# Kernel tuning notes

Hardware: AMD Instinct MI355X
Metric: run time of the kernel (lower is better)

The kernel has to match this reference:

```python
import jax, jax.numpy as jnp
import numpy as np

H, F, E_SHARED, E_ROUTED, K = 1024, 4096, 1, 8, 2


def setup_inputs() -> dict:
    key = jax.random.key(0)
    ks = jax.random.split(key, 6)
    x = jax.random.normal(ks[0], (4, 2048, H), dtype=jnp.float32)
    s = 0.02
    shared_up = jax.random.normal(ks[1], (E_SHARED, H, F), dtype=jnp.float32) * s
    shared_down = jax.random.normal(ks[2], (E_SHARED, F, H), dtype=jnp.float32) * s
    routed_up = jax.random.normal(ks[3], (E_ROUTED, H, F), dtype=jnp.float32) * s
    routed_down = jax.random.normal(ks[4], (E_ROUTED, F, H), dtype=jnp.float32) * s
    router_w = jax.random.normal(ks[5], (H, E_ROUTED), dtype=jnp.float32) * s
    return {"x": x, "shared_up": shared_up, "shared_down": shared_down,
            "routed_up": routed_up, "routed_down": routed_down, "router_w": router_w}


def _expert(x, w_up, w_down):
    # ExpertBlock: down(gelu(up(x))), exact (erf) gelu as in torch F.gelu default
    h = jax.nn.gelu(jnp.einsum('bsh,hf->bsf', x, w_up), approximate=False)
    return jnp.einsum('bsf,fh->bsh', h, w_down)


def reference(x, shared_up, shared_down, routed_up, routed_down, router_w):
    # shared experts (always active)
    shared_out = jnp.zeros_like(x)
    for i in range(E_SHARED):
        shared_out = shared_out + _expert(x, shared_up[i], shared_down[i])

    # router: softmax over routed experts, then top-k gating
    probs = jax.nn.softmax(jnp.einsum('bsh,he->bse', x, router_w), axis=-1)
    top_k_prob, top_k_idx = jax.lax.top_k(probs, K)  # [B,S,K]
    # per-expert gate = sum of top-k probs assigned to that expert
    onehot = jax.nn.one_hot(top_k_idx, E_ROUTED, dtype=x.dtype)  # [B,S,K,E]
    gates = jnp.einsum('bsk,bske->bse', top_k_prob, onehot)      # [B,S,E]

    routed_out = jnp.zeros_like(x)
    for e in range(E_ROUTED):  # fixed small loop over experts
        y = _expert(x, routed_up[e], routed_down[e])
        routed_out = routed_out + gates[..., e:e + 1] * y

    return shared_out + routed_out + x
```

## Files before the change

### kernel.cpp

```cpp
#include <hip/hip_runtime.h>
#include <cstdint>
#include <cstddef>

#define HD 1024
#define FF 4096
#define TOK 8192
#define NSEG 9
#define ROWS_ROUTED (TOK*2)
#define ROWS_TOT (ROWS_ROUTED + TOK)

typedef __bf16 bf16;
typedef __bf16 bf16x8 __attribute__((ext_vector_type(8)));
typedef __bf16 bf16x4 __attribute__((ext_vector_type(4)));
typedef float  f32x4  __attribute__((ext_vector_type(4)));

__device__ __forceinline__ void stage16(const void* g, void* l) {
  __builtin_amdgcn_global_load_lds((const __attribute__((address_space(1))) void*)g,
                                   (__attribute__((address_space(3))) void*)l,
                                   16, 0, 0);
}

__device__ __forceinline__ unsigned short bf_bits(float v) {
  bf16 b = (bf16)v;
  return __builtin_bit_cast(unsigned short, b);
}

__device__ __forceinline__ int xcd_remap(int d) {
  return (((d >> 6) << 3) + (d & 7)) * 8 + ((d >> 3) & 7);
}

__global__ void k_init_meta(int* meta) {
  int t = threadIdx.x;
  if (t < 64) meta[t] = 0;
}

__global__ void k_convert_x(const float* __restrict__ x, bf16* __restrict__ xbf) {
  int i = blockIdx.x*256 + threadIdx.x;
  float4 v = reinterpret_cast<const float4*>(x)[i];
  ushort4 u;
  u.x = bf_bits(v.x); u.y = bf_bits(v.y); u.z = bf_bits(v.z); u.w = bf_bits(v.w);
  reinterpret_cast<ushort4*>(xbf)[i] = u;
}

__global__ void k_tcvt(const float* __restrict__ routed, const float* __restrict__ shared_,
                       bf16* __restrict__ dst, int R, int C) {
  int e = blockIdx.z;
  const float* src = (e < 8) ? (routed + (size_t)e*R*C) : shared_;
  bf16* d = dst + (size_t)e*R*C;
  __shared__ float lds[64][65];
  int r0 = blockIdx.y*64, c0 = blockIdx.x*64;
  int t = threadIdx.x;
  int tr = t>>4, tc4 = (t&15)*4;
  #pragma unroll
  for (int i=0;i<4;i++) {
    float4 v = *reinterpret_cast<const float4*>(src + (size_t)(r0+tr+i*16)*C + c0 + tc4);
    lds[tr+i*16][tc4+0]=v.x; lds[tr+i*16][tc4+1]=v.y;
    lds[tr+i*16][tc4+2]=v.z; lds[tr+i*16][tc4+3]=v.w;
  }
  __syncthreads();
  #pragma unroll
  for (int i=0;i<4;i++) {
    int oc = tr + i*16;
    ushort4 u;
    u.x = bf_bits(lds[tc4+0][oc]);
    u.y = bf_bits(lds[tc4+1][oc]);
    u.z = bf_bits(lds[tc4+2][oc]);
    u.w = bf_bits(lds[tc4+3][oc]);
    *reinterpret_cast<ushort4*>(d + (size_t)(c0+oc)*R + r0 + tc4) = u;
  }
}

__global__ void k_router(const float* __restrict__ x, const float* __restrict__ rw,
                         int* __restrict__ rtE, float* __restrict__ rtG,
                         int* __restrict__ meta) {
  __shared__ float rwl[HD*8];
  int t = threadIdx.x;
  for (int i=t;i<HD*8/4;i+=256)
    reinterpret_cast<float4*>(rwl)[i] = reinterpret_cast<const float4*>(rw)[i];
  __syncthreads();
  int wv = t>>6, lane = t&63;
  int tk = blockIdx.x*4 + wv;
  const float* xr = x + (size_t)tk*HD;
  float a[8] = {0,0,0,0,0,0,0,0};
  for (int i=0;i<HD/64;i++) {
    int h = lane + i*64;
    float xv = xr[h];
    const float* r = rwl + h*8;
    #pragma unroll
    for (int e=0;e<8;e++) a[e] = fmaf(xv, r[e], a[e]);
  }
  #pragma unroll
  for (int e=0;e<8;e++) {
    for (int s=32;s>0;s>>=1) a[e] += __shfl_xor(a[e], s, 64);
  }
  if (lane==0) {
    float mx = a[0];
    #pragma unroll
    for (int e=1;e<8;e++) mx = fmaxf(mx, a[e]);
    float p[8]; float den = 0.f;
    #pragma unroll
    for (int e=0;e<8;e++) { p[e] = expf(a[e]-mx); den += p[e]; }
    int i0 = 0;
    #pragma unroll
    for (int e=1;e<8;e++) if (p[e] > p[i0]) i0 = e;
    int i1 = (i0==0)?1:0;
    #pragma unroll
    for (int e=0;e<8;e++) if (e!=i0 && p[e] > p[i1]) i1 = e;
    float inv = 1.f/den;
    rtE[tk*2] = i0; rtE[tk*2+1] = i1;
    rtG[tk*2] = p[i0]*inv; rtG[tk*2+1] = p[i1]*inv;
    atomicAdd(&meta[i0], 1);
    atomicAdd(&meta[i1], 1);
  }
}

__global__ void k_prefix(int* meta) {
  if (threadIdx.x == 0) {
    int off = 0;
    for (int e=0;e<8;e++) { meta[16+e] = off; meta[32+e] = meta[e]; off += meta[e]; }
    meta[16+8] = ROWS_ROUTED;
    meta[32+8] = TOK;
  }
}

__global__ void k_scatter(const int* __restrict__ rtE, const float* __restrict__ rtG,
                          int* __restrict__ meta, int* __restrict__ tok,
                          float* __restrict__ gate, int* __restrict__ trow) {
  int t = blockIdx.x*256 + threadIdx.x;
  int e0 = rtE[t*2], e1 = rtE[t*2+1];
  float g0 = rtG[t*2], g1 = rtG[t*2+1];
  int p0 = atomicAdd(&meta[8+e0], 1);
  int r0 = meta[16+e0] + p0;
  tok[r0] = t; gate[r0] = g0; trow[t*2] = r0;
  int p1 = atomicAdd(&meta[8+e1], 1);
  int r1 = meta[16+e1] + p1;
  tok[r1] = t; gate[r1] = g1; trow[t*2+1] = r1;
  tok[ROWS_ROUTED + t] = t; gate[ROWS_ROUTED + t] = 1.0f;
}

__global__ void k_combine(const float* __restrict__ x, const bf16* __restrict__ dbuf,
                          const int* __restrict__ trow, float* __restrict__ out) {
  int tkn = blockIdx.x;
  int t = threadIdx.x;
  int r0 = trow[tkn*2], r1 = trow[tkn*2+1];
  int h = t*4;
  float4 xv = *reinterpret_cast<const float4*>(x + (size_t)tkn*HD + h);
  bf16x4 a = *reinterpret_cast<const bf16x4*>(dbuf + (size_t)(ROWS_ROUTED+tkn)*HD + h);
  bf16x4 b = *reinterpret_cast<const bf16x4*>(dbuf + (size_t)r0*HD + h);
  bf16x4 c = *reinterpret_cast<const bf16x4*>(dbuf + (size_t)r1*HD + h);
  float4 o;
  o.x = xv.x + (float)a[0] + (float)b[0] + (float)c[0];
  o.y = xv.y + (float)a[1] + (float)b[1] + (float)c[1];
  o.z = xv.z + (float)a[2] + (float)b[2] + (float)c[2];
  o.w = xv.w + (float)a[3] + (float)b[3] + (float)c[3];
  *reinterpret_cast<float4*>(out + (size_t)tkn*HD + h) = o;
}


#define NKU (HD/32)
#define NKD (FF/32)

__global__ __launch_bounds__(256,3) void k_gemm_up(
    const bf16* __restrict__ xbf, const bf16* __restrict__ wupT,
    bf16* __restrict__ hbuf, const int* __restrict__ tok,
    const int* __restrict__ meta)
{
  int bx = xcd_remap(blockIdx.x);
  int seg = bx >> 11;
  int rem = bx & 2047;
  int mt = rem >> 5, nt = rem & 31;
  int rows = (seg<8)? meta[32+seg] : TOK;
  if (mt*128 >= rows) return;
  int segoff = meta[16+seg];
  int rowbase = mt*128;

  __shared__ __align__(16) bf16 Alds[3][128*32];
  __shared__ __align__(16) bf16 Blds[3][128*32];

  const int t = threadIdx.x;
  const int lane = t & 63, w = t >> 6;

  int lr0 = t>>2, lr1 = 64 + (t>>2);
  int gr0 = rowbase + lr0; if (gr0 >= rows) gr0 = rowbase;
  int gr1 = rowbase + lr1; if (gr1 >= rows) gr1 = rowbase;
  int tok0 = tok[segoff + gr0], tok1 = tok[segoff + gr1];
  int kswz = ((t&3) ^ ((t>>3)&3)) * 8;
  const bf16* gA0 = xbf + (size_t)tok0*HD + kswz;
  const bf16* gA1 = xbf + (size_t)tok1*HD + kswz;
  const bf16* wb = wupT + (size_t)seg*FF*HD;
  int f0 = nt*128;
  const bf16* gB0 = wb + (size_t)(f0 + lr0)*HD + kswz;
  const bf16* gB1 = wb + (size_t)(f0 + lr1)*HD + kswz;

  char* AldsB = (char*)Alds; char* BldsB = (char*)Blds;
  const int stoff = w*1024;

  const int slotb = ((lane>>4) ^ (((lane&15)>>1)&3)) * 16;
  const int Afo = ((w>>1)*64 + (lane&15))*64 + slotb;
  const int Bfo = ((w&1)*64 + (lane&15))*64 + slotb;

  f32x4 acc[4][4] = {};

  stage16(gA0,    AldsB + stoff); stage16(gA1,    AldsB + 4096 + stoff);
  stage16(gB0,    BldsB + stoff); stage16(gB1,    BldsB + 4096 + stoff);
  stage16(gA0+32, AldsB + 8192 + stoff); stage16(gA1+32, AldsB + 12288 + stoff);
  stage16(gB0+32, BldsB + 8192 + stoff); stage16(gB1+32, BldsB + 12288 + stoff);
  __syncthreads();

  int cur = 0;
  for (int kt = 0; kt < NKU; ++kt) {
    if (kt + 2 < NKU) {
      int st = (cur >= 1) ? cur - 1 : 2;
      int ko = (kt+2)*32;
      char* an = AldsB + st*8192; char* bn = BldsB + st*8192;
      stage16(gA0+ko, an + stoff); stage16(gA1+ko, an + 4096 + stoff);
      stage16(gB0+ko, bn + stoff); stage16(gB1+ko, bn + 4096 + stoff);
    }
    const char* Ab = AldsB + cur*8192 + Afo;
    const char* Bb = BldsB + cur*8192 + Bfo;
    bf16x8 af[4], bfr[4];
    #pragma unroll
    for (int m=0;m<4;m++) af[m]  = *reinterpret_cast<const bf16x8*>(Ab + m*1024);
    #pragma unroll
    for (int n=0;n<4;n++) bfr[n] = *reinterpret_cast<const bf16x8*>(Bb + n*1024);
    __builtin_amdgcn_s_setprio(1);
    #pragma unroll
    for (int m=0;m<4;m++)
      #pragma unroll
      for (int n=0;n<4;n++)
        acc[m][n] = __builtin_amdgcn_mfma_f32_16x16x32_bf16(bfr[n], af[m], acc[m][n], 0,0,0);
    __builtin_amdgcn_s_setprio(0);
    if (kt + 2 < NKU)      asm volatile("s_waitcnt vmcnt(8)" ::: "memory");
    else if (kt + 1 < NKU) asm volatile("s_waitcnt vmcnt(0)" ::: "memory");
    if (kt + 1 < NKU) __builtin_amdgcn_s_barrier();
    cur = (cur >= 2) ? 0 : cur + 1;
  }

  const int lrm = lane&15, lq = lane>>4;
  #pragma unroll
  for (int m=0;m<4;m++) {
    int rl = (w>>1)*64 + m*16 + lrm;
    int gr = rowbase + rl;
    if (gr >= rows) continue;
    bf16* hrow = hbuf + (size_t)(segoff+gr)*FF + nt*128 + (w&1)*64 + lq*4;
    #pragma unroll
    for (int n=0;n<4;n++) {
      bf16x4 u;
      #pragma unroll
      for (int j=0;j<4;j++) {
        float v = acc[m][n][j];
        v = 0.5f*v*(1.0f + erff(v*0.70710678118654752f));
        u[j] = (bf16)v;
      }
      *reinterpret_cast<bf16x4*>(hrow + n*16) = u;
    }
  }
}

__global__ __launch_bounds__(256,3) void k_gemm_down(
    const bf16* __restrict__ hbuf, const bf16* __restrict__ wdnT,
    bf16* __restrict__ dbuf, const float* __restrict__ gate,
    const int* __restrict__ meta)
{
  int bx = xcd_remap(blockIdx.x);
  int seg = bx >> 9;
  int rem = bx & 511;
  int mt = rem >> 3, nt = rem & 7;
  int rows = (seg<8)? meta[32+seg] : TOK;
  if (mt*128 >= rows) return;
  int segoff = meta[16+seg];
  int rowbase = mt*128;

  __shared__ __align__(16) bf16 Alds[3][128*32];
  __shared__ __align__(16) bf16 Blds[3][128*32];
  __shared__ float gateL[128];

  const int t = threadIdx.x;
  const int lane = t & 63, w = t >> 6;

  if (t < 128) {
    int gr = rowbase + t; if (gr >= rows) gr = rows - 1;
    gateL[t] = gate[segoff + gr];
  }

  int lr0 = t>>2, lr1 = 64 + (t>>2);
  int kswz = ((t&3) ^ ((t>>3)&3)) * 8;
  const bf16* gA0 = hbuf + (size_t)(segoff + rowbase + lr0)*FF + kswz;
  const bf16* gA1 = hbuf + (size_t)(segoff + rowbase + lr1)*FF + kswz;
  const bf16* wb = wdnT + (size_t)seg*HD*FF;
  int h0 = nt*128;
  const bf16* gB0 = wb + (size_t)(h0 + lr0)*FF + kswz;
  const bf16* gB1 = wb + (size_t)(h0 + lr1)*FF + kswz;

  char* AldsB = (char*)Alds; char* BldsB = (char*)Blds;
  const int stoff = w*1024;

  const int slotb = ((lane>>4) ^ (((lane&15)>>1)&3)) * 16;
  const int Afo = ((w>>1)*64 + (lane&15))*64 + slotb;
  const int Bfo = ((w&1)*64 + (lane&15))*64 + slotb;

  f32x4 acc[4][4] = {};

  stage16(gA0,    AldsB + stoff); stage16(gA1,    AldsB + 4096 + stoff);
  stage16(gB0,    BldsB + stoff); stage16(gB1,    BldsB + 4096 + stoff);
  stage16(gA0+32, AldsB + 8192 + stoff); stage16(gA1+32, AldsB + 12288 + stoff);
  stage16(gB0+32, BldsB + 8192 + stoff); stage16(gB1+32, BldsB + 12288 + stoff);
  __syncthreads();

  int cur = 0;
  for (int kt = 0; kt < NKD; ++kt) {
    if (kt + 2 < NKD) {
      int st = (cur >= 1) ? cur - 1 : 2;
      int ko = (kt+2)*32;
      char* an = AldsB + st*8192; char* bn = BldsB + st*8192;
      stage16(gA0+ko, an + stoff); stage16(gA1+ko, an + 4096 + stoff);
      stage16(gB0+ko, bn + stoff); stage16(gB1+ko, bn + 4096 + stoff);
    }
    const char* Ab = AldsB + cur*8192 + Afo;
    const char* Bb = BldsB + cur*8192 + Bfo;
    bf16x8 af[4], bfr[4];
    #pragma unroll
    for (int m=0;m<4;m++) af[m]  = *reinterpret_cast<const bf16x8*>(Ab + m*1024);
    #pragma unroll
    for (int n=0;n<4;n++) bfr[n] = *reinterpret_cast<const bf16x8*>(Bb + n*1024);
    __builtin_amdgcn_s_setprio(1);
    #pragma unroll
    for (int m=0;m<4;m++)
      #pragma unroll
      for (int n=0;n<4;n++)
        acc[m][n] = __builtin_amdgcn_mfma_f32_16x16x32_bf16(bfr[n], af[m], acc[m][n], 0,0,0);
    __builtin_amdgcn_s_setprio(0);
    if (kt + 2 < NKD)      asm volatile("s_waitcnt vmcnt(8)" ::: "memory");
    else if (kt + 1 < NKD) asm volatile("s_waitcnt vmcnt(0)" ::: "memory");
    if (kt + 1 < NKD) __builtin_amdgcn_s_barrier();
    cur = (cur >= 2) ? 0 : cur + 1;
  }

  const int lrm = lane&15, lq = lane>>4;
  #pragma unroll
  for (int m=0;m<4;m++) {
    int rl = (w>>1)*64 + m*16 + lrm;
    int gr = rowbase + rl;
    if (gr >= rows) continue;
    float g = gateL[rl];
    bf16* drow = dbuf + (size_t)(segoff+gr)*HD + nt*128 + (w&1)*64 + lq*4;
    #pragma unroll
    for (int n=0;n<4;n++) {
      bf16x4 u;
      #pragma unroll
      for (int j=0;j<4;j++) u[j] = (bf16)(acc[m][n][j]*g);
      *reinterpret_cast<bf16x4*>(drow + n*16) = u;
    }
  }
}

struct Layout {
  size_t xbf, wupT, wdnT, hbuf, dbuf, tok, gate, trow, rtE, rtG, meta, total;
};

static inline Layout make_layout() {
  Layout L; size_t o = 0;
  auto al = [&](size_t b){ o = (o+255)&~(size_t)255; size_t r=o; o+=b; return r; };
  L.xbf  = al((size_t)TOK*HD*2);
  L.wupT = al((size_t)NSEG*FF*HD*2);
  L.wdnT = al((size_t)NSEG*FF*HD*2);
  L.hbuf = al((size_t)ROWS_TOT*FF*2);
  L.dbuf = al((size_t)ROWS_TOT*HD*2);
  L.tok  = al((size_t)ROWS_TOT*4);
  L.gate = al((size_t)ROWS_TOT*4);
  L.trow = al((size_t)TOK*2*4);
  L.rtE  = al((size_t)TOK*2*4);
  L.rtG  = al((size_t)TOK*2*4);
  L.meta = al(256*4);
  L.total = o;
  return L;
}

extern "C" void kernel_launch(void* const* d_in, const int* in_sizes, int n_in,
                              void* d_out, int out_size, void* d_ws, size_t ws_size,
                              hipStream_t stream) {
  const float* x           = (const float*)d_in[0];
  const float* shared_up   = (const float*)d_in[1];
  const float* shared_down = (const float*)d_in[2];
  const float* routed_up   = (const float*)d_in[3];
  const float* routed_down = (const float*)d_in[4];
  const float* router_w    = (const float*)d_in[5];
  float* out = (float*)d_out;

  Layout L = make_layout();
  char* ws = (char*)d_ws;
  bf16*  xbf  = (bf16*)(ws + L.xbf);
  bf16*  wupT = (bf16*)(ws + L.wupT);
  bf16*  wdnT = (bf16*)(ws + L.wdnT);
  bf16*  hbuf = (bf16*)(ws + L.hbuf);
  bf16*  dbuf = (bf16*)(ws + L.dbuf);
  int*   tok  = (int*)(ws + L.tok);
  float* gate = (float*)(ws + L.gate);
  int*   trow = (int*)(ws + L.trow);
  int*   rtE  = (int*)(ws + L.rtE);
  float* rtG  = (float*)(ws + L.rtG);
  int*   meta = (int*)(ws + L.meta);

  k_init_meta<<<1, 64, 0, stream>>>(meta);
  k_convert_x<<<TOK*HD/1024, 256, 0, stream>>>(x, xbf);
  k_tcvt<<<dim3(FF/64, HD/64, NSEG), 256, 0, stream>>>(routed_up, shared_up, wupT, HD, FF);
  k_tcvt<<<dim3(HD/64, FF/64, NSEG), 256, 0, stream>>>(routed_down, shared_down, wdnT, FF, HD);
  k_router<<<TOK/4, 256, 0, stream>>>(x, router_w, rtE, rtG, meta);
  k_prefix<<<1, 64, 0, stream>>>(meta);
  k_scatter<<<TOK/256, 256, 0, stream>>>(rtE, rtG, meta, tok, gate, trow);

  k_gemm_up<<<NSEG*64*32, 256, 0, stream>>>(xbf, wupT, hbuf, tok, meta);
  k_gemm_down<<<NSEG*64*8, 256, 0, stream>>>(hbuf, wdnT, dbuf, gate, meta);
  k_combine<<<TOK, 256, 0, stream>>>(x, dbuf, trow, out);
}
```

Baseline: 1.046 ms.

## Use 256x128 GEMM tiles with 512-thread blocks and fuse conversion kernels

Both expert GEMMs move from 128x128 tiles with 256 threads to 256x128 tiles with 512 threads (8 waves). Each B tile is now shared by twice as many rows, which cuts weight traffic per output and lowers the per-thread stage count. The x bf16 conversion is folded into the router kernel, and the two weight transpose-convert launches are merged into one, removing launches and one pass over x. Costs: larger tiles waste more work on the last partial M tile of each expert segment, the grid has half as many blocks, the setprio hints are dropped, and LDS per block rises to about 72KB, which may limit occupancy.

```diff
diff --git a/kernel.cpp b/kernel.cpp
--- a/kernel.cpp
+++ b/kernel.cpp
@@ -34,21 +34,19 @@
   if (t < 64) meta[t] = 0;
 }
 
-__global__ void k_convert_x(const float* __restrict__ x, bf16* __restrict__ xbf) {
-  int i = blockIdx.x*256 + threadIdx.x;
-  float4 v = reinterpret_cast<const float4*>(x)[i];
-  ushort4 u;
-  u.x = bf_bits(v.x); u.y = bf_bits(v.y); u.z = bf_bits(v.z); u.w = bf_bits(v.w);
-  reinterpret_cast<ushort4*>(xbf)[i] = u;
-}
-
-__global__ void k_tcvt(const float* __restrict__ routed, const float* __restrict__ shared_,
-                       bf16* __restrict__ dst, int R, int C) {
-  int e = blockIdx.z;
-  const float* src = (e < 8) ? (routed + (size_t)e*R*C) : shared_;
-  bf16* d = dst + (size_t)e*R*C;
+__global__ void k_tcvt(const float* __restrict__ routed_up, const float* __restrict__ shared_up,
+                       const float* __restrict__ routed_dn, const float* __restrict__ shared_dn,
+                       bf16* __restrict__ wupT, bf16* __restrict__ wdnT) {
+  int z = blockIdx.z;
+  bool isup = z < 9;
+  int e = isup ? z : z - 9;
+  const float* src = isup ? ((e < 8) ? (routed_up + (size_t)e*HD*FF) : shared_up)
+                          : ((e < 8) ? (routed_dn + (size_t)e*FF*HD) : shared_dn);
+  bf16* d = (isup ? wupT : wdnT) + (size_t)e*FF*HD;
+  int R = isup ? HD : FF, C = isup ? FF : HD;
+  int r0 = (isup ? blockIdx.y : blockIdx.x) * 64;
+  int c0 = (isup ? blockIdx.x : blockIdx.y) * 64;
   __shared__ float lds[64][65];
-  int r0 = blockIdx.y*64, c0 = blockIdx.x*64;
   int t = threadIdx.x;
   int tr = t>>4, tc4 = (t&15)*4;
   #pragma unroll
@@ -71,6 +69,7 @@
 }
 
 __global__ void k_router(const float* __restrict__ x, const float* __restrict__ rw,
+                         bf16* __restrict__ xbf,
                          int* __restrict__ rtE, float* __restrict__ rtG,
                          int* __restrict__ meta) {
   __shared__ float rwl[HD*8];
@@ -81,10 +80,12 @@
   int wv = t>>6, lane = t&63;
   int tk = blockIdx.x*4 + wv;
   const float* xr = x + (size_t)tk*HD;
+  bf16* xb = xbf + (size_t)tk*HD;
   float a[8] = {0,0,0,0,0,0,0,0};
   for (int i=0;i<HD/64;i++) {
     int h = lane + i*64;
     float xv = xr[h];
+    xb[h] = (bf16)xv;
     const float* r = rwl + h*8;
     #pragma unroll
     for (int e=0;e<8;e++) a[e] = fmaf(xv, r[e], a[e]);
@@ -157,80 +158,72 @@
 }
 
 
+#define BUFSZ 24576
 #define NKU (HD/32)
 #define NKD (FF/32)
 
-__global__ __launch_bounds__(256,3) void k_gemm_up(
+__global__ __launch_bounds__(512,4) void k_gemm_up(
     const bf16* __restrict__ xbf, const bf16* __restrict__ wupT,
     bf16* __restrict__ hbuf, const int* __restrict__ tok,
     const int* __restrict__ meta)
 {
   int bx = xcd_remap(blockIdx.x);
-  int seg = bx >> 11;
-  int rem = bx & 2047;
+  int seg = bx >> 10;
+  int rem = bx & 1023;
   int mt = rem >> 5, nt = rem & 31;
   int rows = (seg<8)? meta[32+seg] : TOK;
-  if (mt*128 >= rows) return;
+  if (mt*256 >= rows) return;
   int segoff = meta[16+seg];
-  int rowbase = mt*128;
-
-  __shared__ __align__(16) bf16 Alds[3][128*32];
-  __shared__ __align__(16) bf16 Blds[3][128*32];
+  int rowbase = mt*256;
+
+  __shared__ __align__(16) char lds[3*BUFSZ];
 
   const int t = threadIdx.x;
   const int lane = t & 63, w = t >> 6;
-
-  int lr0 = t>>2, lr1 = 64 + (t>>2);
-  int gr0 = rowbase + lr0; if (gr0 >= rows) gr0 = rowbase;
-  int gr1 = rowbase + lr1; if (gr1 >= rows) gr1 = rowbase;
-  int tok0 = tok[segoff + gr0], tok1 = tok[segoff + gr1];
+  const int wm = w >> 1, wn = w & 1;
+
+  int ar = t>>2;
   int kswz = ((t&3) ^ ((t>>3)&3)) * 8;
-  const bf16* gA0 = xbf + (size_t)tok0*HD + kswz;
-  const bf16* gA1 = xbf + (size_t)tok1*HD + kswz;
+  int gr0 = rowbase + ar;        if (gr0 >= rows) gr0 = rows-1;
+  int gr1 = rowbase + 128 + ar;  if (gr1 >= rows) gr1 = rows-1;
+  const bf16* gA0 = xbf + (size_t)tok[segoff+gr0]*HD + kswz;
+  const bf16* gA1 = xbf + (size_t)tok[segoff+gr1]*HD + kswz;
   const bf16* wb = wupT + (size_t)seg*FF*HD;
-  int f0 = nt*128;
-  const bf16* gB0 = wb + (size_t)(f0 + lr0)*HD + kswz;
-  const bf16* gB1 = wb + (size_t)(f0 + lr1)*HD + kswz;
-
-  char* AldsB = (char*)Alds; char* BldsB = (char*)Blds;
-  const int stoff = w*1024;
-
-  const int slotb = ((lane>>4) ^ (((lane&15)>>1)&3)) * 16;
-  const int Afo = ((w>>1)*64 + (lane&15))*64 + slotb;
-  const int Bfo = ((w&1)*64 + (lane&15))*64 + slotb;
+  const bf16* gB = wb + (size_t)(nt*128 + ar)*HD + kswz;
+  const int dA0 = t*16, dA1 = 8192 + t*16, dB = 16384 + t*16;
+
+  const int sx = ((lane>>4) ^ (((lane&15)>>1)&3)) * 16;
+  const int Afo = (wm*64 + (lane&15))*64 + sx;
+  const int Bfo = 16384 + (wn*64 + (lane&15))*64 + sx;
 
   f32x4 acc[4][4] = {};
 
-  stage16(gA0,    AldsB + stoff); stage16(gA1,    AldsB + 4096 + stoff);
-  stage16(gB0,    BldsB + stoff); stage16(gB1,    BldsB + 4096 + stoff);
-  stage16(gA0+32, AldsB + 8192 + stoff); stage16(gA1+32, AldsB + 12288 + stoff);
-  stage16(gB0+32, BldsB + 8192 + stoff); stage16(gB1+32, BldsB + 12288 + stoff);
-  __syncthreads();
+  stage16(gA0,    lds + dA0); stage16(gA1,    lds + dA1); stage16(gB,    lds + dB);
+  stage16(gA0+32, lds + BUFSZ + dA0); stage16(gA1+32, lds + BUFSZ + dA1);
+  stage16(gB+32,  lds + BUFSZ + dB);
+  asm volatile("s_waitcnt vmcnt(3)" ::: "memory");
+  __builtin_amdgcn_s_barrier();
 
   int cur = 0;
   for (int kt = 0; kt < NKU; ++kt) {
     if (kt + 2 < NKU) {
       int st = (cur >= 1) ? cur - 1 : 2;
       int ko = (kt+2)*32;
-      char* an = AldsB + st*8192; char* bn = BldsB + st*8192;
-      stage16(gA0+ko, an + stoff); stage16(gA1+ko, an + 4096 + stoff);
-      stage16(gB0+ko, bn + stoff); stage16(gB1+ko, bn + 4096 + stoff);
+      char* nb = lds + st*BUFSZ;
+      stage16(gA0+ko, nb + dA0); stage16(gA1+ko, nb + dA1); stage16(gB+ko, nb + dB);
     }
-    const char* Ab = AldsB + cur*8192 + Afo;
-    const char* Bb = BldsB + cur*8192 + Bfo;
+    const char* cb = lds + cur*BUFSZ;
     bf16x8 af[4], bfr[4];
     #pragma unroll
-    for (int m=0;m<4;m++) af[m]  = *reinterpret_cast<const bf16x8*>(Ab + m*1024);
-    #pragma unroll
-    for (int n=0;n<4;n++) bfr[n] = *reinterpret_cast<const bf16x8*>(Bb + n*1024);
-    __builtin_amdgcn_s_setprio(1);
+    for (int m=0;m<4;m++) af[m]  = *reinterpret_cast<const bf16x8*>(cb + Afo + m*1024);
+    #pragma unroll
+    for (int n=0;n<4;n++) bfr[n] = *reinterpret_cast<const bf16x8*>(cb + Bfo + n*1024);
     #pragma unroll
     for (int m=0;m<4;m++)
       #pragma unroll
       for (int n=0;n<4;n++)
         acc[m][n] = __builtin_amdgcn_mfma_f32_16x16x32_bf16(bfr[n], af[m], acc[m][n], 0,0,0);
-    __builtin_amdgcn_s_setprio(0);
-    if (kt + 2 < NKU)      asm volatile("s_waitcnt vmcnt(8)" ::: "memory");
+    if (kt + 2 < NKU)      asm volatile("s_waitcnt vmcnt(3)" ::: "memory");
     else if (kt + 1 < NKU) asm volatile("s_waitcnt vmcnt(0)" ::: "memory");
     if (kt + 1 < NKU) __builtin_amdgcn_s_barrier();
     cur = (cur >= 2) ? 0 : cur + 1;
@@ -239,10 +232,10 @@
   const int lrm = lane&15, lq = lane>>4;
   #pragma unroll
   for (int m=0;m<4;m++) {
-    int rl = (w>>1)*64 + m*16 + lrm;
+    int rl = wm*64 + m*16 + lrm;
     int gr = rowbase + rl;
     if (gr >= rows) continue;
-    bf16* hrow = hbuf + (size_t)(segoff+gr)*FF + nt*128 + (w&1)*64 + lq*4;
+    bf16* hrow = hbuf + (size_t)(segoff+gr)*FF + nt*128 + wn*64 + lq*4;
     #pragma unroll
     for (int n=0;n<4;n++) {
       bf16x4 u;
@@ -257,80 +250,72 @@
   }
 }
 
-__global__ __launch_bounds__(256,3) void k_gemm_down(
+__global__ __launch_bounds__(512,4) void k_gemm_down(
     const bf16* __restrict__ hbuf, const bf16* __restrict__ wdnT,
     bf16* __restrict__ dbuf, const float* __restrict__ gate,
     const int* __restrict__ meta)
 {
   int bx = xcd_remap(blockIdx.x);
-  int seg = bx >> 9;
-  int rem = bx & 511;
+  int seg = bx >> 8;
+  int rem = bx & 255;
   int mt = rem >> 3, nt = rem & 7;
   int rows = (seg<8)? meta[32+seg] : TOK;
-  if (mt*128 >= rows) return;
+  if (mt*256 >= rows) return;
   int segoff = meta[16+seg];
-  int rowbase = mt*128;
-
-  __shared__ __align__(16) bf16 Alds[3][128*32];
-  __shared__ __align__(16) bf16 Blds[3][128*32];
-  __shared__ float gateL[128];
+  int rowbase = mt*256;
+
+  __shared__ __align__(16) char lds[3*BUFSZ];
+  __shared__ float gateL[256];
 
   const int t = threadIdx.x;
   const int lane = t & 63, w = t >> 6;
-
-  if (t < 128) {
+  const int wm = w >> 1, wn = w & 1;
+
+  if (t < 256) {
     int gr = rowbase + t; if (gr >= rows) gr = rows - 1;
     gateL[t] = gate[segoff + gr];
   }
 
-  int lr0 = t>>2, lr1 = 64 + (t>>2);
+  int ar = t>>2;
   int kswz = ((t&3) ^ ((t>>3)&3)) * 8;
-  const bf16* gA0 = hbuf + (size_t)(segoff + rowbase + lr0)*FF + kswz;
-  const bf16* gA1 = hbuf + (size_t)(segoff + rowbase + lr1)*FF + kswz;
+  const bf16* gA0 = hbuf + (size_t)(segoff + rowbase + ar)*FF + kswz;
+  const bf16* gA1 = hbuf + (size_t)(segoff + rowbase + 128 + ar)*FF + kswz;
   const bf16* wb = wdnT + (size_t)seg*HD*FF;
-  int h0 = nt*128;
-  const bf16* gB0 = wb + (size_t)(h0 + lr0)*FF + kswz;
-  const bf16* gB1 = wb + (size_t)(h0 + lr1)*FF + kswz;
-
-  char* AldsB = (char*)Alds; char* BldsB = (char*)Blds;
-  const int stoff = w*1024;
-
-  const int slotb = ((lane>>4) ^ (((lane&15)>>1)&3)) * 16;
-  const int Afo = ((w>>1)*64 + (lane&15))*64 + slotb;
-  const int Bfo = ((w&1)*64 + (lane&15))*64 + slotb;
+  const bf16* gB = wb + (size_t)(nt*128 + ar)*FF + kswz;
+  const int dA0 = t*16, dA1 = 8192 + t*16, dB = 16384 + t*16;
+
+  const int sx = ((lane>>4) ^ (((lane&15)>>1)&3)) * 16;
+  const int Afo = (wm*64 + (lane&15))*64 + sx;
+  const int Bfo = 16384 + (wn*64 + (lane&15))*64 + sx;
 
   f32x4 acc[4][4] = {};
 
-  stage16(gA0,    AldsB + stoff); stage16(gA1,    AldsB + 4096 + stoff);
-  stage16(gB0,    BldsB + stoff); stage16(gB1,    BldsB + 4096 + stoff);
-  stage16(gA0+32, AldsB + 8192 + stoff); stage16(gA1+32, AldsB + 12288 + stoff);
-  stage16(gB0+32, BldsB + 8192 + stoff); stage16(gB1+32, BldsB + 12288 + stoff);
-  __syncthreads();
+  stage16(gA0,    lds + dA0); stage16(gA1,    lds + dA1); stage16(gB,    lds + dB);
+  stage16(gA0+32, lds + BUFSZ + dA0); stage16(gA1+32, lds + BUFSZ + dA1);
+  stage16(gB+32,  lds + BUFSZ + dB);
+  asm volatile("s_waitcnt vmcnt(3)" ::: "memory");
+  __builtin_amdgcn_s_barrier();
 
   int cur = 0;
   for (int kt = 0; kt < NKD; ++kt) {
     if (kt + 2 < NKD) {
       int st = (cur >= 1) ? cur - 1 : 2;
       int ko = (kt+2)*32;
-      char* an = AldsB + st*8192; char* bn = BldsB + st*8192;
-      stage16(gA0+ko, an + stoff); stage16(gA1+ko, an + 4096 + stoff);
-      stage16(gB0+ko, bn + stoff); stage16(gB1+ko, bn + 4096 + stoff);
+      char* nb = lds + st*BUFSZ;
+      stage16(gA0+ko, nb + dA0); stage16(gA1+ko, nb + dA1); stage16(gB+ko, nb + dB);
     }
-    const char* Ab = AldsB + cur*8192 + Afo;
-    const char* Bb = BldsB + cur*8192 + Bfo;
+    const char* cb = lds + cur*BUFSZ;
     bf16x8 af[4], bfr[4];
     #pragma unroll
-    for (int m=0;m<4;m++) af[m]  = *reinterpret_cast<const bf16x8*>(Ab + m*1024);
-    #pragma unroll
-    for (int n=0;n<4;n++) bfr[n] = *reinterpret_cast<const bf16x8*>(Bb + n*1024);
-    __builtin_amdgcn_s_setprio(1);
+    for (int m=0;m<4;m++) af[m]  = *reinterpret_cast<const bf16x8*>(cb + Afo + m*1024);
+    #pragma unroll
+    for (int n=0;n<4;n++) bfr[n] = *reinterpret_cast<const bf16x8*>(cb + Bfo + n*1024);
     #pragma unroll
     for (int m=0;m<4;m++)
       #pragma unroll
       for (int n=0;n<4;n++)
         acc[m][n] = __builtin_amdgcn_mfma_f32_16x16x32_bf16(bfr[n], af[m], acc[m][n], 0,0,0);
-    __builtin_amdgcn_s_setprio(0);
-    if (kt + 2 < NKD)      asm volatile("s_waitcnt vmcnt(8)" ::: "memory");
+    if (kt + 2 < NKD)      asm volatile("s_waitcnt vmcnt(3)" ::: "memory");
     else if (kt + 1 < NKD) asm volatile("s_waitcnt vmcnt(0)" ::: "memory");
     if (kt + 1 < NKD) __builtin_amdgcn_s_barrier();
     cur = (cur >= 2) ? 0 : cur + 1;
@@ -339,11 +324,11 @@
   const int lrm = lane&15, lq = lane>>4;
   #pragma unroll
   for (int m=0;m<4;m++) {
-    int rl = (w>>1)*64 + m*16 + lrm;
+    int rl = wm*64 + m*16 + lrm;
     int gr = rowbase + rl;
     if (gr >= rows) continue;
     float g = gateL[rl];
-    bf16* drow = dbuf + (size_t)(segoff+gr)*HD + nt*128 + (w&1)*64 + lq*4;
+    bf16* drow = dbuf + (size_t)(segoff+gr)*HD + nt*128 + wn*64 + lq*4;
     #pragma unroll
     for (int n=0;n<4;n++) {
       bf16x4 u;
@@ -402,14 +387,12 @@
   int*   meta = (int*)(ws + L.meta);
 
   k_init_meta<<<1, 64, 0, stream>>>(meta);
-  k_convert_x<<<TOK*HD/1024, 256, 0, stream>>>(x, xbf);
-  k_tcvt<<<dim3(FF/64, HD/64, NSEG), 256, 0, stream>>>(routed_up, shared_up, wupT, HD, FF);
-  k_tcvt<<<dim3(HD/64, FF/64, NSEG), 256, 0, stream>>>(routed_down, shared_down, wdnT, FF, HD);
-  k_router<<<TOK/4, 256, 0, stream>>>(x, router_w, rtE, rtG, meta);
+  k_tcvt<<<dim3(64, 16, 18), 256, 0, stream>>>(routed_up, shared_up, routed_down, shared_down, wupT, wdnT);
+  k_router<<<TOK/4, 256, 0, stream>>>(x, router_w, xbf, rtE, rtG, meta);
   k_prefix<<<1, 64, 0, stream>>>(meta);
   k_scatter<<<TOK/256, 256, 0, stream>>>(rtE, rtG, meta, tok, gate, trow);
 
-  k_gemm_up<<<NSEG*64*32, 256, 0, stream>>>(xbf, wupT, hbuf, tok, meta);
-  k_gemm_down<<<NSEG*64*8, 256, 0, stream>>>(hbuf, wdnT, dbuf, gate, meta);
+  k_gemm_up<<<NSEG*32*32, 512, 0, stream>>>(xbf, wupT, hbuf, tok, meta);
+  k_gemm_down<<<NSEG*32*8, 512, 0, stream>>>(hbuf, wdnT, dbuf, gate, meta);
   k_combine<<<TOK, 256, 0, stream>>>(x, dbuf, trow, out);
 }
```

Result: faster. 988.8 us (-5.5%).
